# Optimization experiments

Measured on AMD Instinct MI355X. Metric: run time of the kernel, lower is better.

The kernel has to match this reference:

```python
import jax, jax.numpy as jnp
import numpy as np
import math

B, S, D, H = 2, 2048, 1024, 16
DK = D // H
THETA = 10000.0

def _rope_tables(seq_len, dk, theta):
    freqs = 1.0 / theta ** (np.arange(0, dk, 2)[: dk // 2].astype(np.float32) / dk)
    t = np.arange(seq_len, dtype=np.float32)
    ang = np.outer(t, freqs)  # [S, dk/2]
    return jnp.asarray(np.cos(ang)), jnp.asarray(np.sin(ang))

def setup_inputs() -> dict:
    key = jax.random.key(0)
    ks = jax.random.split(key, 12)
    init = lambda k, shape: (0.02 * jax.random.normal(k, shape)).astype(jnp.float32)
    cos, sin = _rope_tables(S, DK, THETA)
    mask = jnp.tril(jnp.ones((S, S), dtype=jnp.int32))[None, None]  # [1,1,S,S] causal
    return {
        'Q': jax.random.normal(ks[0], (B, S, D), jnp.float32),
        'K': jax.random.normal(ks[1], (B, S, D), jnp.float32),
        'V': jax.random.normal(ks[2], (B, S, D), jnp.float32),
        'mask': mask,
        'Wq_w': init(ks[3], (D, D)), 'Wq_b': init(ks[4], (D,)),
        'Wk_w': init(ks[5], (D, D)), 'Wk_b': init(ks[6], (D,)),
        'Wv_w': init(ks[7], (D, D)), 'Wv_b': init(ks[8], (D,)),
        'Wo_w': init(ks[9], (D, D)), 'Wo_b': init(ks[10], (D,)),
        'cos': cos, 'sin': sin,
    }

def _apply_rope(x, cos, sin):
    # x: [B, S, H, DK]; cos/sin: [S, DK/2]
    x1 = x[..., 0::2]
    x2 = x[..., 1::2]
    c = cos[None, :, None, :]
    s = sin[None, :, None, :]
    out_even = x1 * c - x2 * s
    out_odd = x1 * s + x2 * c
    return jnp.stack([out_even, out_odd], axis=-1).reshape(x.shape)

def reference(Q, K, V, mask, Wq_w, Wq_b, Wk_w, Wk_b, Wv_w, Wv_b, Wo_w, Wo_b, cos, sin):
    b, s, d = Q.shape
    q = (Q @ Wq_w.T + Wq_b).reshape(b, s, H, DK)
    k = (K @ Wk_w.T + Wk_b).reshape(b, s, H, DK)
    v = (V @ Wv_w.T + Wv_b).reshape(b, s, H, DK)
    q = _apply_rope(q, cos[:s], sin[:s])
    k = _apply_rope(k, cos[:s], sin[:s])
    # [B,H,S,DK]
    q = q.transpose(0, 2, 1, 3)
    k = k.transpose(0, 2, 1, 3)
    v = v.transpose(0, 2, 1, 3)
    scores = jnp.einsum('bhqd,bhkd->bhqk', q, k) / math.sqrt(DK)
    scores = jnp.where(mask == 0, jnp.float32(-1e9), scores)
    probs = jax.nn.softmax(scores, axis=-1)
    out = jnp.einsum('bhqk,bhkd->bhqd', probs, v)  # [B,H,S,DK]
    out = out.transpose(0, 2, 1, 3).reshape(b, s, d)
    return out @ Wo_w.T + Wo_b
```

## Files before the change

### kernel.cpp

```cpp
#include <hip/hip_runtime.h>
#include <cstdint>
#include <cstddef>


typedef __bf16 bf16x8 __attribute__((ext_vector_type(8)));
typedef float floatx4 __attribute__((ext_vector_type(4)));

#define DI __device__ __forceinline__

DI unsigned short f2bf(float f) {
  union { float f; unsigned int u; } v; v.f = f;
  unsigned int r = v.u + 0x7fffu + ((v.u >> 16) & 1u);
  return (unsigned short)(r >> 16);
}

DI unsigned short bfb(float f) {
  __bf16 h = (__bf16)f;
  union { __bf16 h; unsigned short u; } c; c.h = h;
  return c.u;
}

DI void async_ld16(const void* g, void* l) {
  __builtin_amdgcn_global_load_lds(
      (const __attribute__((address_space(1))) unsigned int*)g,
      (__attribute__((address_space(3))) unsigned int*)l, 16, 0, 0);
}

__global__ void cvt_all(const float* __restrict__ Q, const float* __restrict__ K,
                        const float* __restrict__ V, const float* __restrict__ Wq,
                        const float* __restrict__ Wk, const float* __restrict__ Wv,
                        const float* __restrict__ Wo, unsigned short* __restrict__ dst) {
  int i = blockIdx.x * blockDim.x + threadIdx.x;
  const float* s;
  int off;
  if (i < 3145728) {
    if (i < 1048576) { s = Q; off = i; }
    else if (i < 2097152) { s = K; off = i - 1048576; }
    else { s = V; off = i - 2097152; }
  } else {
    int j = i - 3145728;
    int wsel = j >> 18;
    off = j & 262143;
    s = (wsel == 0) ? Wq : (wsel == 1) ? Wk : (wsel == 2) ? Wv : Wo;
  }
  float4 f = reinterpret_cast<const float4*>(s)[off];
  ushort4 o;
  o.x = f2bf(f.x); o.y = f2bf(f.y); o.z = f2bf(f.z); o.w = f2bf(f.w);
  reinterpret_cast<ushort4*>(dst)[i] = o;
}

__global__ __launch_bounds__(256)
void gemm_qkv(const unsigned short* __restrict__ Qb, const unsigned short* __restrict__ Kb,
              const unsigned short* __restrict__ Vb, const unsigned short* __restrict__ Wq,
              const unsigned short* __restrict__ Wk, const unsigned short* __restrict__ Wv,
              const float* __restrict__ bq, const float* __restrict__ bk,
              const float* __restrict__ bv, unsigned short* __restrict__ qh,
              unsigned short* __restrict__ kh, unsigned short* __restrict__ vtp,
              const float* __restrict__ cosT, const float* __restrict__ sinT) {
  __shared__ unsigned short As[128 * 32];
  __shared__ unsigned short Bs[128 * 32];

  const int proj = blockIdx.x >> 3;
  const unsigned short* X = (proj == 0) ? Qb : (proj == 1) ? Kb : Vb;
  const unsigned short* W = (proj == 0) ? Wq : (proj == 1) ? Wk : Wv;
  const float* bias = (proj == 0) ? bq : (proj == 1) ? bk : bv;
  unsigned short* outB = (proj == 0) ? qh : (proj == 1) ? kh : vtp;

  const int t = threadIdx.x;
  const int lane = t & 63;
  const int w = t >> 6;
  const int row0 = blockIdx.y * 128;
  const int col0 = (blockIdx.x & 7) * 128;
  const int wm = (w >> 1) * 64;
  const int wn = (w & 1) * 64;
  const int fr = lane & 15;
  const int fk = (lane >> 4) * 8;
  const int rbase = (lane >> 4) * 4;

  floatx4 acc[4][4];
#pragma unroll
  for (int i = 0; i < 4; ++i)
#pragma unroll
    for (int j = 0; j < 4; ++j)
      acc[i][j] = (floatx4){0.f, 0.f, 0.f, 0.f};

  for (int k0 = 0; k0 < 1024; k0 += 32) {
    __syncthreads();
#pragma unroll
    for (int it = 0; it < 2; ++it) {
      int c = it * 256 + t;
      int r = c >> 2, cc = c & 3;
      async_ld16(X + (size_t)(row0 + r) * 1024 + k0 + cc * 8, &As[c * 8]);
    }
#pragma unroll
    for (int it = 0; it < 2; ++it) {
      int c = it * 256 + t;
      int r = c >> 2, cc = c & 3;
      async_ld16(W + (size_t)(col0 + r) * 1024 + k0 + cc * 8, &Bs[c * 8]);
    }
    __syncthreads();

    bf16x8 af[4], bfr[4];
#pragma unroll
    for (int i = 0; i < 4; ++i)
      af[i] = *reinterpret_cast<const bf16x8*>(&As[(wm + i * 16 + fr) * 32 + fk]);
#pragma unroll
    for (int j = 0; j < 4; ++j)
      bfr[j] = *reinterpret_cast<const bf16x8*>(&Bs[(wn + j * 16 + fr) * 32 + fk]);
#pragma unroll
    for (int i = 0; i < 4; ++i)
#pragma unroll
      for (int j = 0; j < 4; ++j)
        acc[i][j] = __builtin_amdgcn_mfma_f32_16x16x32_bf16(af[i], bfr[j], acc[i][j], 0, 0, 0);
  }

#pragma unroll
  for (int j = 0; j < 4; ++j) {
    const int col = col0 + wn + j * 16 + fr;
    const float bvv = bias[col];
#pragma unroll
    for (int i = 0; i < 4; ++i) {
#pragma unroll
      for (int r = 0; r < 4; ++r) {
        const int row = row0 + wm + i * 16 + rbase + r;
        float v = acc[i][j][r] + bvv;
        const int bb = row >> 11, sp = row & 2047, hh = col >> 6, dk = col & 63;
        if (proj < 2) {
          float p = __shfl_xor(v, 1);
          const int i2 = (col & 63) >> 1;
          const float cv = cosT[sp * 32 + i2];
          const float sv = sinT[sp * 32 + i2];
          float res = ((col & 1) == 0) ? (v * cv - p * sv) : (p * sv + v * cv);
          if (proj == 0) res *= 0.125f;
          outB[(((size_t)(bb * 16 + hh)) * 2048 + sp) * 64 + dk] = f2bf(res);
        } else {
          outB[(((size_t)(bb * 16 + hh)) * 64 + dk) * 2048 + sp] = f2bf(v);
        }
      }
    }
  }
}

__global__ __launch_bounds__(256)
void gemm_out(const unsigned short* __restrict__ X, const unsigned short* __restrict__ W,
              const float* __restrict__ bias, float* __restrict__ outF) {
  __shared__ unsigned short As[64 * 32];
  __shared__ unsigned short Bs[128 * 32];

  const int t = threadIdx.x;
  const int lane = t & 63;
  const int w = t >> 6;
  const int row0 = blockIdx.y * 64;
  const int col0 = blockIdx.x * 128;
  const int wm = (w >> 1) * 32;
  const int wn = (w & 1) * 64;
  const int fr = lane & 15;
  const int fk = (lane >> 4) * 8;
  const int rbase = (lane >> 4) * 4;

  floatx4 acc[2][4];
#pragma unroll
  for (int i = 0; i < 2; ++i)
#pragma unroll
    for (int j = 0; j < 4; ++j)
      acc[i][j] = (floatx4){0.f, 0.f, 0.f, 0.f};

  for (int k0 = 0; k0 < 1024; k0 += 32) {
    __syncthreads();
    {
      int c = t;
      int r = c >> 2, cc = c & 3;
      async_ld16(X + (size_t)(row0 + r) * 1024 + k0 + cc * 8, &As[c * 8]);
    }
#pragma unroll
    for (int it = 0; it < 2; ++it) {
      int c = it * 256 + t;
      int r = c >> 2, cc = c & 3;
      async_ld16(W + (size_t)(col0 + r) * 1024 + k0 + cc * 8, &Bs[c * 8]);
    }
    __syncthreads();

    bf16x8 af[2], bfr[4];
#pragma unroll
    for (int i = 0; i < 2; ++i)
      af[i] = *reinterpret_cast<const bf16x8*>(&As[(wm + i * 16 + fr) * 32 + fk]);
#pragma unroll
    for (int j = 0; j < 4; ++j)
      bfr[j] = *reinterpret_cast<const bf16x8*>(&Bs[(wn + j * 16 + fr) * 32 + fk]);
#pragma unroll
    for (int i = 0; i < 2; ++i)
#pragma unroll
      for (int j = 0; j < 4; ++j)
        acc[i][j] = __builtin_amdgcn_mfma_f32_16x16x32_bf16(af[i], bfr[j], acc[i][j], 0, 0, 0);
  }

#pragma unroll
  for (int j = 0; j < 4; ++j) {
    const int col = col0 + wn + j * 16 + fr;
    const float bvv = bias[col];
#pragma unroll
    for (int i = 0; i < 2; ++i)
#pragma unroll
      for (int r = 0; r < 4; ++r) {
        const int row = row0 + wm + i * 16 + rbase + r;
        outF[(size_t)row * 1024 + col] = acc[i][j][r] + bvv;
      }
  }
}

__global__ __launch_bounds__(256)
void flash_attn(const unsigned short* __restrict__ qh,
                const unsigned short* __restrict__ kh,
                const unsigned short* __restrict__ vt,
                unsigned short* __restrict__ out) {
  __shared__ unsigned short Ks[2][64 * 64];
  __shared__ unsigned short Vs[2][64 * 64];
  __shared__ unsigned short Ps[8][16 * 64];

  const int t = threadIdx.x, lane = t & 63, w = t >> 6;
  const int g = lane >> 4;
  const int fr = lane & 15;
  const int fk = g * 8;
  const int rbase = g * 4;
  const int bh = blockIdx.y;
  const int qbA = blockIdx.x;
  const int qbB = 31 - qbA;
  const int qwA = qbA * 64 + w * 16;
  const int qwB = qbB * 64 + w * 16;

  const size_t baseQK = (size_t)bh * 2048 * 64;
  const size_t baseV = (size_t)bh * 64 * 2048;

  bf16x8 qfA[2], qfB[2];
  qfA[0] = *reinterpret_cast<const bf16x8*>(&qh[baseQK + (size_t)(qwA + fr) * 64 + fk]);
  qfA[1] = *reinterpret_cast<const bf16x8*>(&qh[baseQK + (size_t)(qwA + fr) * 64 + 32 + fk]);
  qfB[0] = *reinterpret_cast<const bf16x8*>(&qh[baseQK + (size_t)(qwB + fr) * 64 + fk]);
  qfB[1] = *reinterpret_cast<const bf16x8*>(&qh[baseQK + (size_t)(qwB + fr) * 64 + 32 + fk]);

  floatx4 oA[4], oB[4];
  float lA[4], lB[4];
#pragma unroll
  for (int i = 0; i < 4; ++i) {
    oA[i] = (floatx4){0.f, 0.f, 0.f, 0.f};
    oB[i] = (floatx4){0.f, 0.f, 0.f, 0.f};
    lA[i] = 0.f; lB[i] = 0.f;
  }

  auto stage = [&](int kb, int buf) {
    const int k0 = kb * 64;
#pragma unroll
    for (int it = 0; it < 2; ++it) {
      int c = it * 256 + t;
      int r = c >> 3, cg = (c & 7) ^ (r & 7);
      async_ld16(kh + baseQK + (size_t)(k0 + r) * 64 + cg * 8, &Ks[buf][c * 8]);
    }
#pragma unroll
    for (int it = 0; it < 2; ++it) {
      int c = it * 256 + t;
      int r = c >> 3, cg = (c & 7) ^ (r & 7);
      async_ld16(vt + baseV + (size_t)r * 2048 + k0 + cg * 8, &Vs[buf][c * 8]);
    }
  };

  const int nkb = qbB + 1;
  stage(0, 0);
  __syncthreads();

  for (int kb = 0; kb < nkb; ++kb) {
    const int cur = kb & 1;
    if (kb + 1 < nkb) stage(kb + 1, cur ^ 1);
    const int k0 = kb * 64;
    const bool aAct = (kb <= qbA);

    bf16x8 kf[4][2];
#pragma unroll
    for (int j = 0; j < 4; ++j)
#pragma unroll
      for (int kk = 0; kk < 2; ++kk)
        kf[j][kk] = *reinterpret_cast<const bf16x8*>(
            &Ks[cur][(j * 16 + fr) * 64 + ((((kk << 2) | g) ^ (fr & 7)) << 3)]);

    floatx4 sB[4], sA[4];
#pragma unroll
    for (int j = 0; j < 4; ++j) {
      sB[j] = (floatx4){0.f, 0.f, 0.f, 0.f};
      sA[j] = (floatx4){0.f, 0.f, 0.f, 0.f};
    }
#pragma unroll
    for (int j = 0; j < 4; ++j)
#pragma unroll
      for (int kk = 0; kk < 2; ++kk)
        sB[j] = __builtin_amdgcn_mfma_f32_16x16x32_bf16(qfB[kk], kf[j][kk], sB[j], 0, 0, 0);
    if (aAct) {
#pragma unroll
      for (int j = 0; j < 4; ++j)
#pragma unroll
        for (int kk = 0; kk < 2; ++kk)
          sA[j] = __builtin_amdgcn_mfma_f32_16x16x32_bf16(qfA[kk], kf[j][kk], sA[j], 0, 0, 0);
    }

    if (k0 + 63 > qwB) {
#pragma unroll
      for (int j = 0; j < 4; ++j)
#pragma unroll
        for (int r = 0; r < 4; ++r)
          if (k0 + j * 16 + fr > qwB + rbase + r) sB[j][r] = -1e30f;
    }
    if (aAct && k0 + 63 > qwA) {
#pragma unroll
      for (int j = 0; j < 4; ++j)
#pragma unroll
        for (int r = 0; r < 4; ++r)
          if (k0 + j * 16 + fr > qwA + rbase + r) sA[j][r] = -1e30f;
    }

#pragma unroll
    for (int j = 0; j < 4; ++j) {
      const int chb = (j * 16 + fr) >> 3;
      const int cin = fr & 7;
#pragma unroll
      for (int r = 0; r < 4; ++r) {
        const int row = rbase + r;
        float pB = __expf(sB[j][r]);
        lB[r] += pB;
        Ps[w][row * 64 + ((chb ^ (row & 7)) << 3) + cin] = bfb(pB);
      }
    }
    if (aAct) {
#pragma unroll
      for (int j = 0; j < 4; ++j) {
        const int chb = (j * 16 + fr) >> 3;
        const int cin = fr & 7;
#pragma unroll
        for (int r = 0; r < 4; ++r) {
          const int row = rbase + r;
          float pA = __expf(sA[j][r]);
          lA[r] += pA;
          Ps[w + 4][row * 64 + ((chb ^ (row & 7)) << 3) + cin] = bfb(pA);
        }
      }
    }

    bf16x8 vf[4][2], pB2[2], pA2[2];
#pragma unroll
    for (int id = 0; id < 4; ++id)
#pragma unroll
      for (int kk = 0; kk < 2; ++kk)
        vf[id][kk] = *reinterpret_cast<const bf16x8*>(
            &Vs[cur][(id * 16 + fr) * 64 + ((((kk << 2) | g) ^ (fr & 7)) << 3)]);
#pragma unroll
    for (int kk = 0; kk < 2; ++kk)
      pB2[kk] = *reinterpret_cast<const bf16x8*>(
          &Ps[w][fr * 64 + ((((kk << 2) | g) ^ (fr & 7)) << 3)]);
#pragma unroll
    for (int kk = 0; kk < 2; ++kk)
#pragma unroll
      for (int id = 0; id < 4; ++id)
        oB[id] = __builtin_amdgcn_mfma_f32_16x16x32_bf16(pB2[kk], vf[id][kk], oB[id], 0, 0, 0);
    if (aAct) {
#pragma unroll
      for (int kk = 0; kk < 2; ++kk)
        pA2[kk] = *reinterpret_cast<const bf16x8*>(
            &Ps[w + 4][fr * 64 + ((((kk << 2) | g) ^ (fr & 7)) << 3)]);
#pragma unroll
      for (int kk = 0; kk < 2; ++kk)
#pragma unroll
        for (int id = 0; id < 4; ++id)
          oA[id] = __builtin_amdgcn_mfma_f32_16x16x32_bf16(pA2[kk], vf[id][kk], oA[id], 0, 0, 0);
    }

    __syncthreads();
  }

#pragma unroll
  for (int r = 0; r < 4; ++r) {
#pragma unroll
    for (int d = 1; d < 16; d <<= 1) {
      lB[r] += __shfl_xor(lB[r], d);
      lA[r] += __shfl_xor(lA[r], d);
    }
  }

  const int bb = bh >> 4, hh = bh & 15;
#pragma unroll
  for (int id = 0; id < 4; ++id)
#pragma unroll
    for (int r = 0; r < 4; ++r) {
      const int qrA = qwA + rbase + r;
      const int qrB = qwB + rbase + r;
      out[((size_t)(bb * 2048 + qrA)) * 1024 + hh * 64 + id * 16 + fr] = bfb(oA[id][r] / lA[r]);
      out[((size_t)(bb * 2048 + qrB)) * 1024 + hh * 64 + id * 16 + fr] = bfb(oB[id][r] / lB[r]);
    }
}

extern "C" void kernel_launch(void* const* d_in, const int* in_sizes, int n_in,
                              void* d_out, int out_size, void* d_ws, size_t ws_size,
                              hipStream_t stream) {
  const float* Q  = (const float*)d_in[0];
  const float* K  = (const float*)d_in[1];
  const float* V  = (const float*)d_in[2];
  const float* Wq = (const float*)d_in[4];
  const float* bq = (const float*)d_in[5];
  const float* Wk = (const float*)d_in[6];
  const float* bk = (const float*)d_in[7];
  const float* Wv = (const float*)d_in[8];
  const float* bv = (const float*)d_in[9];
  const float* Wo = (const float*)d_in[10];
  const float* bo = (const float*)d_in[11];
  const float* cosT = (const float*)d_in[12];
  const float* sinT = (const float*)d_in[13];

  char* ws = (char*)d_ws;
  const size_t MB = 1024 * 1024;
  unsigned short* Qb  = (unsigned short*)(ws + 0 * MB);
  unsigned short* Kb  = (unsigned short*)(ws + 8 * MB);
  unsigned short* Vb  = (unsigned short*)(ws + 16 * MB);
  unsigned short* Wqb = (unsigned short*)(ws + 24 * MB);
  unsigned short* Wkb = (unsigned short*)(ws + 26 * MB);
  unsigned short* Wvb = (unsigned short*)(ws + 28 * MB);
  unsigned short* Wob = (unsigned short*)(ws + 30 * MB);
  unsigned short* qh  = (unsigned short*)(ws + 32 * MB);
  unsigned short* khp = (unsigned short*)(ws + 40 * MB);
  unsigned short* vtp = (unsigned short*)(ws + 48 * MB);
  unsigned short* ao  = (unsigned short*)(ws + 56 * MB);

  cvt_all<<<16384, 256, 0, stream>>>(Q, K, V, Wq, Wk, Wv, Wo, (unsigned short*)ws);

  gemm_qkv<<<dim3(24, 32), 256, 0, stream>>>(Qb, Kb, Vb, Wqb, Wkb, Wvb, bq, bk, bv,
                                             qh, khp, vtp, cosT, sinT);
  flash_attn<<<dim3(16, 32), 256, 0, stream>>>(qh, khp, vtp, ao);
  gemm_out<<<dim3(8, 64), 256, 0, stream>>>(ao, Wob, bo, (float*)d_out);
}
```

Before: 283.1 us.

## Double-buffer GEMM LDS tiles, remap block order, and transpose V-projection MFMA for coalesced stores

Both projection GEMMs now double-buffer their LDS tiles, so the next K-slice's async global-to-LDS load is issued before the MFMAs on the current slice, with one barrier per iteration instead of two. Grids are flattened to 1D and block IDs are remapped so that consecutive blocks share the same weight column tile, which improves L2 reuse. For the V projection the MFMA operands are swapped so the accumulator holds the transposed tile, letting the transposed V stores run along the sequence dimension and coalesce. This doubles LDS use, and there is a possible race on the async LDS writes if the single barrier does not order the outstanding global_load_lds operations.

```diff
diff --git a/kernel.cpp b/kernel.cpp
--- a/kernel.cpp
+++ b/kernel.cpp
@@ -57,10 +57,15 @@
               const float* __restrict__ bv, unsigned short* __restrict__ qh,
               unsigned short* __restrict__ kh, unsigned short* __restrict__ vtp,
               const float* __restrict__ cosT, const float* __restrict__ sinT) {
-  __shared__ unsigned short As[128 * 32];
-  __shared__ unsigned short Bs[128 * 32];
-
-  const int proj = blockIdx.x >> 3;
+  __shared__ unsigned short As[2][128 * 32];
+  __shared__ unsigned short Bs[2][128 * 32];
+
+  const int id = blockIdx.x;
+  const int xb = id / 96;
+  const int rem = id - xb * 96;
+  const int proj = rem >> 5;
+  const int yb = rem & 31;
+
   const unsigned short* X = (proj == 0) ? Qb : (proj == 1) ? Kb : Vb;
   const unsigned short* W = (proj == 0) ? Wq : (proj == 1) ? Wk : Wv;
   const float* bias = (proj == 0) ? bq : (proj == 1) ? bk : bv;
@@ -69,8 +74,8 @@
   const int t = threadIdx.x;
   const int lane = t & 63;
   const int w = t >> 6;
-  const int row0 = blockIdx.y * 128;
-  const int col0 = (blockIdx.x & 7) * 128;
+  const int row0 = yb * 128;
+  const int col0 = xb * 128;
   const int wm = (w >> 1) * 64;
   const int wn = (w & 1) * 64;
   const int fr = lane & 15;
@@ -84,48 +89,63 @@
     for (int j = 0; j < 4; ++j)
       acc[i][j] = (floatx4){0.f, 0.f, 0.f, 0.f};
 
-  for (int k0 = 0; k0 < 1024; k0 += 32) {
-    __syncthreads();
+  auto stage = [&](int k0, int buf) {
 #pragma unroll
     for (int it = 0; it < 2; ++it) {
       int c = it * 256 + t;
       int r = c >> 2, cc = c & 3;
-      async_ld16(X + (size_t)(row0 + r) * 1024 + k0 + cc * 8, &As[c * 8]);
+      async_ld16(X + (size_t)(row0 + r) * 1024 + k0 + cc * 8, &As[buf][c * 8]);
     }
 #pragma unroll
     for (int it = 0; it < 2; ++it) {
       int c = it * 256 + t;
       int r = c >> 2, cc = c & 3;
-      async_ld16(W + (size_t)(col0 + r) * 1024 + k0 + cc * 8, &Bs[c * 8]);
+      async_ld16(W + (size_t)(col0 + r) * 1024 + k0 + cc * 8, &Bs[buf][c * 8]);
+    }
+  };
+
+  stage(0, 0);
+  __syncthreads();
+
+  for (int kb = 0; kb < 32; ++kb) {
+    const int cur = kb & 1;
+    if (kb + 1 < 32) stage((kb + 1) * 32, cur ^ 1);
+
+    bf16x8 af[4], bfr[4];
+#pragma unroll
+    for (int i = 0; i < 4; ++i)
+      af[i] = *reinterpret_cast<const bf16x8*>(&As[cur][(wm + i * 16 + fr) * 32 + fk]);
+#pragma unroll
+    for (int j = 0; j < 4; ++j)
+      bfr[j] = *reinterpret_cast<const bf16x8*>(&Bs[cur][(wn + j * 16 + fr) * 32 + fk]);
+    if (proj == 2) {
+#pragma unroll
+      for (int i = 0; i < 4; ++i)
+#pragma unroll
+        for (int j = 0; j < 4; ++j)
+          acc[i][j] = __builtin_amdgcn_mfma_f32_16x16x32_bf16(bfr[j], af[i], acc[i][j], 0, 0, 0);
+    } else {
+#pragma unroll
+      for (int i = 0; i < 4; ++i)
+#pragma unroll
+        for (int j = 0; j < 4; ++j)
+          acc[i][j] = __builtin_amdgcn_mfma_f32_16x16x32_bf16(af[i], bfr[j], acc[i][j], 0, 0, 0);
     }
     __syncthreads();
-
-    bf16x8 af[4], bfr[4];
-#pragma unroll
-    for (int i = 0; i < 4; ++i)
-      af[i] = *reinterpret_cast<const bf16x8*>(&As[(wm + i * 16 + fr) * 32 + fk]);
-#pragma unroll
-    for (int j = 0; j < 4; ++j)
-      bfr[j] = *reinterpret_cast<const bf16x8*>(&Bs[(wn + j * 16 + fr) * 32 + fk]);
-#pragma unroll
-    for (int i = 0; i < 4; ++i)
-#pragma unroll
-      for (int j = 0; j < 4; ++j)
-        acc[i][j] = __builtin_amdgcn_mfma_f32_16x16x32_bf16(af[i], bfr[j], acc[i][j], 0, 0, 0);
-  }
-
-#pragma unroll
-  for (int j = 0; j < 4; ++j) {
-    const int col = col0 + wn + j * 16 + fr;
-    const float bvv = bias[col];
-#pragma unroll
-    for (int i = 0; i < 4; ++i) {
-#pragma unroll
-      for (int r = 0; r < 4; ++r) {
-        const int row = row0 + wm + i * 16 + rbase + r;
-        float v = acc[i][j][r] + bvv;
-        const int bb = row >> 11, sp = row & 2047, hh = col >> 6, dk = col & 63;
-        if (proj < 2) {
+  }
+
+  if (proj < 2) {
+#pragma unroll
+    for (int j = 0; j < 4; ++j) {
+      const int col = col0 + wn + j * 16 + fr;
+      const float bvv = bias[col];
+#pragma unroll
+      for (int i = 0; i < 4; ++i) {
+#pragma unroll
+        for (int r = 0; r < 4; ++r) {
+          const int row = row0 + wm + i * 16 + rbase + r;
+          float v = acc[i][j][r] + bvv;
+          const int bb = row >> 11, sp = row & 2047, hh = col >> 6, dk = col & 63;
           float p = __shfl_xor(v, 1);
           const int i2 = (col & 63) >> 1;
           const float cv = cosT[sp * 32 + i2];
@@ -133,8 +153,22 @@
           float res = ((col & 1) == 0) ? (v * cv - p * sv) : (p * sv + v * cv);
           if (proj == 0) res *= 0.125f;
           outB[(((size_t)(bb * 16 + hh)) * 2048 + sp) * 64 + dk] = f2bf(res);
-        } else {
-          outB[(((size_t)(bb * 16 + hh)) * 64 + dk) * 2048 + sp] = f2bf(v);
+        }
+      }
+    }
+  } else {
+#pragma unroll
+    for (int j = 0; j < 4; ++j) {
+#pragma unroll
+      for (int r = 0; r < 4; ++r) {
+        const int dkc = col0 + wn + j * 16 + rbase + r;
+        const float bvv = bias[dkc];
+        const int hh = dkc >> 6, dk = dkc & 63;
+#pragma unroll
+        for (int i = 0; i < 4; ++i) {
+          const int spf = row0 + wm + i * 16 + fr;
+          const int bb = spf >> 11, sp = spf & 2047;
+          vtp[(((size_t)(bb * 16 + hh)) * 64 + dk) * 2048 + sp] = f2bf(acc[i][j][r] + bvv);
         }
       }
     }
@@ -144,14 +178,18 @@
 __global__ __launch_bounds__(256)
 void gemm_out(const unsigned short* __restrict__ X, const unsigned short* __restrict__ W,
               const float* __restrict__ bias, float* __restrict__ outF) {
-  __shared__ unsigned short As[64 * 32];
-  __shared__ unsigned short Bs[128 * 32];
+  __shared__ unsigned short As[2][64 * 32];
+  __shared__ unsigned short Bs[2][128 * 32];
+
+  const int id = blockIdx.x;
+  const int xb = id >> 6;
+  const int yb = id & 63;
 
   const int t = threadIdx.x;
   const int lane = t & 63;
   const int w = t >> 6;
-  const int row0 = blockIdx.y * 64;
-  const int col0 = blockIdx.x * 128;
+  const int row0 = yb * 64;
+  const int col0 = xb * 128;
   const int wm = (w >> 1) * 32;
   const int wn = (w & 1) * 64;
   const int fr = lane & 15;
@@ -165,33 +203,40 @@
     for (int j = 0; j < 4; ++j)
       acc[i][j] = (floatx4){0.f, 0.f, 0.f, 0.f};
 
-  for (int k0 = 0; k0 < 1024; k0 += 32) {
-    __syncthreads();
+  auto stage = [&](int k0, int buf) {
     {
       int c = t;
       int r = c >> 2, cc = c & 3;
-      async_ld16(X + (size_t)(row0 + r) * 1024 + k0 + cc * 8, &As[c * 8]);
+      async_ld16(X + (size_t)(row0 + r) * 1024 + k0 + cc * 8, &As[buf][c * 8]);
     }
 #pragma unroll
     for (int it = 0; it < 2; ++it) {
       int c = it * 256 + t;
       int r = c >> 2, cc = c & 3;
-      async_ld16(W + (size_t)(col0 + r) * 1024 + k0 + cc * 8, &Bs[c * 8]);
-    }
-    __syncthreads();
+      async_ld16(W + (size_t)(col0 + r) * 1024 + k0 + cc * 8, &Bs[buf][c * 8]);
+    }
+  };
+
+  stage(0, 0);
+  __syncthreads();
+
+  for (int kb = 0; kb < 32; ++kb) {
+    const int cur = kb & 1;
+    if (kb + 1 < 32) stage((kb + 1) * 32, cur ^ 1);
 
     bf16x8 af[2], bfr[4];
 #pragma unroll
     for (int i = 0; i < 2; ++i)
-      af[i] = *reinterpret_cast<const bf16x8*>(&As[(wm + i * 16 + fr) * 32 + fk]);
-#pragma unroll
-    for (int j = 0; j < 4; ++j)
-      bfr[j] = *reinterpret_cast<const bf16x8*>(&Bs[(wn + j * 16 + fr) * 32 + fk]);
+      af[i] = *reinterpret_cast<const bf16x8*>(&As[cur][(wm + i * 16 + fr) * 32 + fk]);
+#pragma unroll
+    for (int j = 0; j < 4; ++j)
+      bfr[j] = *reinterpret_cast<const bf16x8*>(&Bs[cur][(wn + j * 16 + fr) * 32 + fk]);
 #pragma unroll
     for (int i = 0; i < 2; ++i)
 #pragma unroll
       for (int j = 0; j < 4; ++j)
         acc[i][j] = __builtin_amdgcn_mfma_f32_16x16x32_bf16(af[i], bfr[j], acc[i][j], 0, 0, 0);
+    __syncthreads();
   }
 
 #pragma unroll
@@ -222,8 +267,9 @@
   const int fr = lane & 15;
   const int fk = g * 8;
   const int rbase = g * 4;
-  const int bh = blockIdx.y;
-  const int qbA = blockIdx.x;
+  const int id = blockIdx.x;
+  const int qbA = id >> 5;
+  const int bh = id & 31;
   const int qbB = 31 - qbA;
   const int qwA = qbA * 64 + w * 16;
   const int qwB = qbB * 64 + w * 16;
@@ -343,11 +389,11 @@
 
     bf16x8 vf[4][2], pB2[2], pA2[2];
 #pragma unroll
-    for (int id = 0; id < 4; ++id)
+    for (int id2 = 0; id2 < 4; ++id2)
 #pragma unroll
       for (int kk = 0; kk < 2; ++kk)
-        vf[id][kk] = *reinterpret_cast<const bf16x8*>(
-            &Vs[cur][(id * 16 + fr) * 64 + ((((kk << 2) | g) ^ (fr & 7)) << 3)]);
+        vf[id2][kk] = *reinterpret_cast<const bf16x8*>(
+            &Vs[cur][(id2 * 16 + fr) * 64 + ((((kk << 2) | g) ^ (fr & 7)) << 3)]);
 #pragma unroll
     for (int kk = 0; kk < 2; ++kk)
       pB2[kk] = *reinterpret_cast<const bf16x8*>(
@@ -355,8 +401,8 @@
 #pragma unroll
     for (int kk = 0; kk < 2; ++kk)
 #pragma unroll
-      for (int id = 0; id < 4; ++id)
-        oB[id] = __builtin_amdgcn_mfma_f32_16x16x32_bf16(pB2[kk], vf[id][kk], oB[id], 0, 0, 0);
+      for (int id2 = 0; id2 < 4; ++id2)
+        oB[id2] = __builtin_amdgcn_mfma_f32_16x16x32_bf16(pB2[kk], vf[id2][kk], oB[id2], 0, 0, 0);
     if (aAct) {
 #pragma unroll
       for (int kk = 0; kk < 2; ++kk)
@@ -365,8 +411,8 @@
 #pragma unroll
       for (int kk = 0; kk < 2; ++kk)
 #pragma unroll
-        for (int id = 0; id < 4; ++id)
-          oA[id] = __builtin_amdgcn_mfma_f32_16x16x32_bf16(pA2[kk], vf[id][kk], oA[id], 0, 0, 0);
+        for (int id2 = 0; id2 < 4; ++id2)
+          oA[id2] = __builtin_amdgcn_mfma_f32_16x16x32_bf16(pA2[kk], vf[id2][kk], oA[id2], 0, 0, 0);
     }
 
     __syncthreads();
@@ -383,13 +429,13 @@
 
   const int bb = bh >> 4, hh = bh & 15;
 #pragma unroll
-  for (int id = 0; id < 4; ++id)
+  for (int id2 = 0; id2 < 4; ++id2)
 #pragma unroll
     for (int r = 0; r < 4; ++r) {
       const int qrA = qwA + rbase + r;
       const int qrB = qwB + rbase + r;
-      out[((size_t)(bb * 2048 + qrA)) * 1024 + hh * 64 + id * 16 + fr] = bfb(oA[id][r] / lA[r]);
-      out[((size_t)(bb * 2048 + qrB)) * 1024 + hh * 64 + id * 16 + fr] = bfb(oB[id][r] / lB[r]);
+      out[((size_t)(bb * 2048 + qrA)) * 1024 + hh * 64 + id2 * 16 + fr] = bfb(oA[id2][r] / lA[r]);
+      out[((size_t)(bb * 2048 + qrB)) * 1024 + hh * 64 + id2 * 16 + fr] = bfb(oB[id2][r] / lB[r]);
     }
 }
 
@@ -426,8 +472,8 @@
 
   cvt_all<<<16384, 256, 0, stream>>>(Q, K, V, Wq, Wk, Wv, Wo, (unsigned short*)ws);
 
-  gemm_qkv<<<dim3(24, 32), 256, 0, stream>>>(Qb, Kb, Vb, Wqb, Wkb, Wvb, bq, bk, bv,
-                                             qh, khp, vtp, cosT, sinT);
-  flash_attn<<<dim3(16, 32), 256, 0, stream>>>(qh, khp, vtp, ao);
-  gemm_out<<<dim3(8, 64), 256, 0, stream>>>(ao, Wob, bo, (float*)d_out);
-}
+  gemm_qkv<<<768, 256, 0, stream>>>(Qb, Kb, Vb, Wqb, Wkb, Wvb, bq, bk, bv,
+                                    qh, khp, vtp, cosT, sinT);
+  flash_attn<<<512, 256, 0, stream>>>(qh, khp, vtp, ao);
+  gemm_out<<<512, 256, 0, stream>>>(ao, Wob, bo, (float*)d_out);
+}
```

Result: faster. 260.3 us (-8.0%).
